# Kernel optimization log

Measured on AMD Instinct MI355X. Metric: run time of the kernel, lower is better.

## Reference

```python
import jax, jax.numpy as jnp
import numpy as np

D = 256          # out_feats
H = 4            # n_heads
DH = D // H      # per-head feats
S = 8192         # number of snapshots (segments)
PER = 32         # edges (selected papers) per snapshot
E = S * PER      # total edges
NP = 200000      # number of papers
ST = 10          # snapshot_types (embedding has ST+1 rows, padding_idx=-1)
SLOPE = 0.01     # LeakyReLU negative slope (torch default)


def setup_inputs() -> dict:
    key = jax.random.key(0)
    ks = jax.random.split(key, 20)
    sc = 1.0 / np.sqrt(D)
    papers = jax.random.normal(ks[0], (NP, D), dtype=jnp.float32)
    snapshots = jax.random.normal(ks[1], (S, D), dtype=jnp.float32)
    cur_snapshot_types = jax.random.randint(ks[2], (S,), 0, ST + 1, dtype=jnp.int32)
    is_cite = jax.random.randint(ks[3], (NP,), 0, 2, dtype=jnp.int32)
    selected_indicator = jax.random.randint(ks[4], (E,), 0, NP, dtype=jnp.int64)
    # contiguous sorted segment ids, PER edges per snapshot (matches valid_num_nodes)
    index = jnp.repeat(jnp.arange(S, dtype=jnp.int32), PER)
    # linear layers (torch Linear: y = x @ W.T + b)
    W_src = jax.random.normal(ks[5], (D, D), dtype=jnp.float32) * sc
    b_src = jnp.zeros((D,), dtype=jnp.float32)
    W_dst = jax.random.normal(ks[6], (D, D), dtype=jnp.float32) * sc
    b_dst = jnp.zeros((D,), dtype=jnp.float32)
    W_out = jax.random.normal(ks[7], (D, D), dtype=jnp.float32) * sc
    b_out = jnp.zeros((D,), dtype=jnp.float32)
    # node attr embeddings (2 rows, padding_idx=0 -> row 0 zero)
    emb_cite = jax.random.normal(ks[8], (2, D), dtype=jnp.float32).at[0].set(0.0)
    emb_ref = jax.random.normal(ks[9], (2, D), dtype=jnp.float32).at[0].set(0.0)
    emb_target = jax.random.normal(ks[10], (2, D), dtype=jnp.float32).at[0].set(0.0)
    # snapshot type embedding (ST+1 rows, padding_idx=-1 -> last row zero)
    snapshot_emb = jax.random.normal(ks[11], (ST + 1, D), dtype=jnp.float32).at[-1].set(0.0)
    # attention vectors, xavier_normal with relu gain
    gain = np.sqrt(2.0)
    std = gain * np.sqrt(2.0 / (H * DH + 1))
    attn = jax.random.normal(ks[12], (1, H, DH), dtype=jnp.float32) * std
    attn_t = jax.random.normal(ks[13], (1, H, DH), dtype=jnp.float32) * std
    return {
        "papers": papers, "snapshots": snapshots,
        "W_src": W_src, "b_src": b_src, "W_dst": W_dst, "b_dst": b_dst,
        "W_out": W_out, "b_out": b_out,
        "emb_cite": emb_cite, "emb_ref": emb_ref, "emb_target": emb_target,
        "snapshot_emb": snapshot_emb, "attn": attn, "attn_t": attn_t,
        "cur_snapshot_types": cur_snapshot_types, "is_cite": is_cite,
        "selected_indicator": selected_indicator, "index": index,
    }


def _leaky(x):
    return jnp.where(x >= 0, x, SLOPE * x)


def reference(papers, snapshots, W_src, b_src, W_dst, b_dst, W_out, b_out,
              emb_cite, emb_ref, emb_target, snapshot_emb, attn, attn_t,
              cur_snapshot_types, is_cite, selected_indicator, index):
    # gather src papers per edge: [E, D]
    h_src = papers[selected_indicator]
    feat_src = (h_src @ W_src.T + b_src).reshape(-1, H, DH)          # [E,H,DH]
    ic = is_cite[selected_indicator]
    # original uses 'is_cite' indices for all three attr embeddings (faithful)
    src_type_h = (emb_cite[ic] + emb_ref[ic] + emb_target[ic]).reshape(-1, H, DH)
    dst_type_h = snapshot_emb[cur_snapshot_types].reshape(-1, H, DH)  # [S,H,DH]
    feat_dst = (snapshots @ W_dst.T + b_dst).reshape(-1, H, DH)[index]  # [E,H,DH]
    # per-edge attention logits
    e = (_leaky(feat_src + feat_dst) * attn).sum(axis=-1)             # [E,H]
    et = (_leaky(src_type_h + dst_type_h[index]) * attn_t).sum(axis=-1)
    e = e + et
    # segment (edge) softmax over destination snapshots
    m = jax.lax.stop_gradient(jax.ops.segment_max(e, index, num_segments=S))
    ex = jnp.exp(e - m[index])
    den = jax.ops.segment_sum(ex, index, num_segments=S)
    a = (ex / den[index])[..., None]                                  # [E,H,1]
    # weighted segment-sum aggregation
    x = feat_src * a
    sum_out = jax.ops.segment_sum(x, index, num_segments=S).reshape(S, D)
    return sum_out @ W_out.T + b_out
```

## Files before the change

### kernel.cpp

```cpp
#include <hip/hip_runtime.h>
#include <hip/hip_fp16.h>
#include <type_traits>

#define NSNAP 8192
#define PER 32
#define SLOPE 0.01f

using half8   = __attribute__((ext_vector_type(8))) _Float16;
using floatx4 = __attribute__((ext_vector_type(4))) float;

__device__ __forceinline__ float leaky(float x) { return x >= 0.f ? x : SLOPE * x; }

__device__ __forceinline__ unsigned pack2(float a, float b) {
    __half2 h = __floats2half2_rn(a, b);
    return *reinterpret_cast<unsigned*>(&h);
}

__global__ __launch_bounds__(256) void pack_w(const float* __restrict__ W,
                                              _Float16* __restrict__ Wh) {
    const int i = blockIdx.x * 256 + threadIdx.x;
    const float4 v = *(const float4*)(W + (long)i * 4);
    *(uint2*)(Wh + (long)i * 4) = make_uint2(pack2(v.x, v.y), pack2(v.z, v.w));
}

template <typename AT, typename OT>
__global__ __launch_bounds__(256) void gemm_nt(const AT* __restrict__ A,
                                               const float* __restrict__ W,
                                               const float* __restrict__ bias,
                                               OT* __restrict__ Cout, int M) {
    constexpr int LDA = 40;
    __shared__ _Float16 Asl[128 * LDA];
    __shared__ _Float16 Wsl[128 * LDA];

    const int m0 = blockIdx.x * 128;
    const int n0 = blockIdx.y * 128;
    const int tid = threadIdx.x;
    const int lane = tid & 63;
    const int wave = tid >> 6;
    const int wm = (wave & 1) * 64;
    const int wn = (wave >> 1) * 64;
    const int l15 = lane & 15;
    const int quad = lane >> 4;

    floatx4 acc[4][4];
#pragma unroll
    for (int i = 0; i < 4; i++)
#pragma unroll
        for (int j = 0; j < 4; j++) acc[i][j] = (floatx4)0.f;

    for (int k0 = 0; k0 < 256; k0 += 32) {
        __syncthreads();
#pragma unroll
        for (int it = 0; it < 4; ++it) {
            const int idx = tid + it * 256;
            const int row = idx >> 3;
            const int c4 = idx & 7;
            long gm = (long)m0 + row;
            if (gm >= M) gm = M - 1;
            if constexpr (std::is_same_v<AT, float>) {
                const float4 v = *(const float4*)(A + gm * 256 + k0 + c4 * 4);
                *(uint2*)(&Asl[row * LDA + c4 * 4]) = make_uint2(pack2(v.x, v.y), pack2(v.z, v.w));
            } else {
                const uint2 v = *(const uint2*)(A + gm * 256 + k0 + c4 * 4);
                *(uint2*)(&Asl[row * LDA + c4 * 4]) = v;
            }
            const float4 w = *(const float4*)(W + (long)(n0 + row) * 256 + k0 + c4 * 4);
            *(uint2*)(&Wsl[row * LDA + c4 * 4]) = make_uint2(pack2(w.x, w.y), pack2(w.z, w.w));
        }
        __syncthreads();

        half8 af[4], bf[4];
#pragma unroll
        for (int i = 0; i < 4; i++)
            af[i] = *reinterpret_cast<const half8*>(&Asl[(wm + i * 16 + l15) * LDA + quad * 8]);
#pragma unroll
        for (int j = 0; j < 4; j++)
            bf[j] = *reinterpret_cast<const half8*>(&Wsl[(wn + j * 16 + l15) * LDA + quad * 8]);
#pragma unroll
        for (int i = 0; i < 4; i++)
#pragma unroll
            for (int j = 0; j < 4; j++)
                acc[i][j] = __builtin_amdgcn_mfma_f32_16x16x32_f16(af[i], bf[j], acc[i][j], 0, 0, 0);
    }

#pragma unroll
    for (int j = 0; j < 4; j++) {
        const int gcol = n0 + wn + j * 16 + l15;
        const float bv = bias[gcol];
#pragma unroll
        for (int i = 0; i < 4; i++) {
            const int rbase = m0 + wm + i * 16 + quad * 4;
#pragma unroll
            for (int r = 0; r < 4; r++) {
                const int grow = rbase + r;
                if (grow < M) {
                    const float v = acc[i][j][r] + bv;
                    if constexpr (std::is_same_v<OT, __half>)
                        Cout[(long)grow * 256 + gcol] = __float2half(v);
                    else
                        Cout[(long)grow * 256 + gcol] = v;
                }
            }
        }
    }
}

__global__ __launch_bounds__(256, 2) void fused_attn(
    const float* __restrict__ papers, const _Float16* __restrict__ Wh,
    const float* __restrict__ b_src, const float* __restrict__ F,
    const float* __restrict__ emb_cite, const float* __restrict__ emb_ref,
    const float* __restrict__ emb_target, const float* __restrict__ snap_emb,
    const float* __restrict__ attn, const float* __restrict__ attn_t,
    const int* __restrict__ types, const int* __restrict__ is_cite,
    const int* __restrict__ sel, __half* __restrict__ SO) {
    constexpr int LDA = 40;
    __shared__ _Float16 Asl[64 * LDA];
    __shared__ _Float16 Wsl[256 * LDA];
    __shared__ int ic_l[64];

    const int tid = threadIdx.x;
    const int lane = tid & 63;
    const int wave = tid >> 6;
    const int l15 = lane & 15;
    const int quad = lane >> 4;
    const int sbase = blockIdx.x * 2;
    const int ebase = blockIdx.x * 64;

    if (tid < 64) ic_l[tid] = is_cite[sel[ebase + tid]];

    const int arow_idx = tid >> 2;
    const int ac8 = tid & 3;
    const long arow = (long)sel[ebase + arow_idx];

    floatx4 acc[4][4];
#pragma unroll
    for (int i = 0; i < 4; i++)
#pragma unroll
        for (int j = 0; j < 4; j++) acc[i][j] = (floatx4)0.f;

    for (int k0 = 0; k0 < 256; k0 += 32) {
        __syncthreads();
        const float4 a0 = *(const float4*)(papers + arow * 256 + k0 + ac8 * 8);
        const float4 a1 = *(const float4*)(papers + arow * 256 + k0 + ac8 * 8 + 4);
        *(uint4*)(&Asl[arow_idx * LDA + ac8 * 8]) =
            make_uint4(pack2(a0.x, a0.y), pack2(a0.z, a0.w), pack2(a1.x, a1.y), pack2(a1.z, a1.w));
#pragma unroll
        for (int it = 0; it < 4; ++it) {
            const int task = tid + it * 256;
            const int n = task >> 2;
            const int c = task & 3;
            *(uint4*)(&Wsl[n * LDA + c * 8]) = *(const uint4*)(Wh + n * 256 + k0 + c * 8);
        }
        __syncthreads();

        half8 af[4], bf[4];
#pragma unroll
        for (int i = 0; i < 4; i++)
            af[i] = *reinterpret_cast<const half8*>(&Asl[(i * 16 + l15) * LDA + quad * 8]);
#pragma unroll
        for (int j = 0; j < 4; j++)
            bf[j] = *reinterpret_cast<const half8*>(&Wsl[(64 * wave + j * 16 + l15) * LDA + quad * 8]);
#pragma unroll
        for (int i = 0; i < 4; i++)
#pragma unroll
            for (int j = 0; j < 4; j++)
                acc[i][j] = __builtin_amdgcn_mfma_f32_16x16x32_f16(af[i], bf[j], acc[i][j], 0, 0, 0);
    }

    float bsrc_j[4], attn_j[4], F0_j[4], F1_j[4];
#pragma unroll
    for (int j = 0; j < 4; j++) {
        const int col = 64 * wave + j * 16 + l15;
        bsrc_j[j] = b_src[col];
        attn_j[j] = attn[col];
        F0_j[j] = F[(long)sbase * 256 + col];
        F1_j[j] = F[(long)(sbase + 1) * 256 + col];
    }
#pragma unroll
    for (int i = 0; i < 4; i++)
#pragma unroll
        for (int j = 0; j < 4; j++)
#pragma unroll
            for (int r = 0; r < 4; r++) acc[i][j][r] += bsrc_j[j];

    const int D = 64 * wave + lane;
    const float at_d = attn_t[D];
    const float src0 = emb_cite[D] + emb_ref[D] + emb_target[D];
    const float src1 = emb_cite[256 + D] + emb_ref[256 + D] + emb_target[256 + D];
    float et[2][2];
#pragma unroll
    for (int sn = 0; sn < 2; sn++) {
        const float dstt = snap_emb[types[sbase + sn] * 256 + D];
        float p0 = leaky(src0 + dstt) * at_d;
        float p1 = leaky(src1 + dstt) * at_d;
#pragma unroll
        for (int off = 32; off; off >>= 1) {
            p0 += __shfl_xor(p0, off);
            p1 += __shfl_xor(p1, off);
        }
        et[sn][0] = p0;
        et[sn][1] = p1;
    }

    float lg[4][4];
#pragma unroll
    for (int i = 0; i < 4; i++) {
        const int sn = i >> 1;
#pragma unroll
        for (int r = 0; r < 4; r++) {
            float p = 0.f;
#pragma unroll
            for (int j = 0; j < 4; j++)
                p += leaky(acc[i][j][r] + (sn == 0 ? F0_j[j] : F1_j[j])) * attn_j[j];
#pragma unroll
            for (int off = 1; off <= 8; off <<= 1) p += __shfl_xor(p, off);
            const int row = i * 16 + quad * 4 + r;
            lg[i][r] = p + et[sn][ic_l[row]];
        }
    }

    float aw[4][4];
#pragma unroll
    for (int sn = 0; sn < 2; sn++) {
        float m = -3.4e38f;
#pragma unroll
        for (int ii = 0; ii < 2; ii++)
#pragma unroll
            for (int r = 0; r < 4; r++) m = fmaxf(m, lg[sn * 2 + ii][r]);
        m = fmaxf(m, __shfl_xor(m, 16));
        m = fmaxf(m, __shfl_xor(m, 32));
        float den = 0.f;
#pragma unroll
        for (int ii = 0; ii < 2; ii++)
#pragma unroll
            for (int r = 0; r < 4; r++) {
                const float ex = __expf(lg[sn * 2 + ii][r] - m);
                aw[sn * 2 + ii][r] = ex;
                den += ex;
            }
        den += __shfl_xor(den, 16);
        den += __shfl_xor(den, 32);
        const float inv = 1.f / den;
#pragma unroll
        for (int ii = 0; ii < 2; ii++)
#pragma unroll
            for (int r = 0; r < 4; r++) aw[sn * 2 + ii][r] *= inv;
    }

#pragma unroll
    for (int sn = 0; sn < 2; sn++) {
#pragma unroll
        for (int j = 0; j < 4; j++) {
            float o = 0.f;
#pragma unroll
            for (int ii = 0; ii < 2; ii++)
#pragma unroll
                for (int r = 0; r < 4; r++) o += aw[sn * 2 + ii][r] * acc[sn * 2 + ii][j][r];
            o += __shfl_xor(o, 16);
            o += __shfl_xor(o, 32);
            if (quad == sn)
                SO[(long)(sbase + sn) * 256 + 64 * wave + j * 16 + l15] = __float2half(o);
        }
    }
}

extern "C" void kernel_launch(void* const* d_in, const int* in_sizes, int n_in,
                              void* d_out, int out_size, void* d_ws, size_t ws_size,
                              hipStream_t stream) {
    const float* papers     = (const float*)d_in[0];
    const float* snapshots  = (const float*)d_in[1];
    const float* W_src      = (const float*)d_in[2];
    const float* b_src      = (const float*)d_in[3];
    const float* W_dst      = (const float*)d_in[4];
    const float* b_dst      = (const float*)d_in[5];
    const float* W_out      = (const float*)d_in[6];
    const float* b_out      = (const float*)d_in[7];
    const float* emb_cite   = (const float*)d_in[8];
    const float* emb_ref    = (const float*)d_in[9];
    const float* emb_target = (const float*)d_in[10];
    const float* snap_emb   = (const float*)d_in[11];
    const float* attn       = (const float*)d_in[12];
    const float* attn_t     = (const float*)d_in[13];
    const int* types        = (const int*)d_in[14];
    const int* is_cite      = (const int*)d_in[15];
    const int* sel          = (const int*)d_in[16];

    char* ws = (char*)d_ws;
    float*     F    = (float*)ws;
    __half*    SO   = (__half*)(ws + 8388608);
    _Float16*  Wh   = (_Float16*)(ws + 12582912);

    pack_w<<<64, 256, 0, stream>>>(W_src, Wh);
    gemm_nt<float, float><<<dim3(64, 2), 256, 0, stream>>>(snapshots, W_dst, b_dst, F, NSNAP);
    fused_attn<<<NSNAP / 2, 256, 0, stream>>>(papers, Wh, b_src, F, emb_cite, emb_ref,
                                              emb_target, snap_emb, attn, attn_t, types,
                                              is_cite, sel, SO);
    gemm_nt<__half, float><<<dim3(64, 2), 256, 0, stream>>>(SO, W_out, b_out, (float*)d_out, NSNAP);
}
```

Measured before the change: 414.3 us.

## Prepack W_src in MFMA fragment order and stage full A tile once

```diff
diff --git a/kernel.cpp b/kernel.cpp
--- a/kernel.cpp
+++ b/kernel.cpp
@@ -16,11 +16,18 @@
     return *reinterpret_cast<unsigned*>(&h);
 }
 
-__global__ __launch_bounds__(256) void pack_w(const float* __restrict__ W,
-                                              _Float16* __restrict__ Wh) {
-    const int i = blockIdx.x * 256 + threadIdx.x;
-    const float4 v = *(const float4*)(W + (long)i * 4);
-    *(uint2*)(Wh + (long)i * 4) = make_uint2(pack2(v.x, v.y), pack2(v.z, v.w));
+__global__ __launch_bounds__(256) void pack_w_frag(const float* __restrict__ W,
+                                                   _Float16* __restrict__ Wh) {
+    const int t = blockIdx.x * 256 + threadIdx.x;
+    const int lane = t & 63;
+    const int wj = (t >> 6) & 15;
+    const int k0 = t >> 10;
+    const int n = (wj >> 2) * 64 + (wj & 3) * 16 + (lane & 15);
+    const int k = k0 * 32 + (lane >> 4) * 8;
+    const float4 v0 = *(const float4*)(W + (long)n * 256 + k);
+    const float4 v1 = *(const float4*)(W + (long)n * 256 + k + 4);
+    *(uint4*)(Wh + (long)t * 8) =
+        make_uint4(pack2(v0.x, v0.y), pack2(v0.z, v0.w), pack2(v1.x, v1.y), pack2(v1.z, v1.w));
 }
 
 template <typename AT, typename OT>
@@ -113,9 +120,7 @@
     const float* __restrict__ attn, const float* __restrict__ attn_t,
     const int* __restrict__ types, const int* __restrict__ is_cite,
     const int* __restrict__ sel, __half* __restrict__ SO) {
-    constexpr int LDA = 40;
-    __shared__ _Float16 Asl[64 * LDA];
-    __shared__ _Float16 Wsl[256 * LDA];
+    __shared__ _Float16 Asl[64 * 256];
     __shared__ int ic_l[64];
 
     const int tid = threadIdx.x;
@@ -128,9 +133,24 @@
 
     if (tid < 64) ic_l[tid] = is_cite[sel[ebase + tid]];
 
-    const int arow_idx = tid >> 2;
-    const int ac8 = tid & 3;
-    const long arow = (long)sel[ebase + arow_idx];
+    {
+        const int r = tid >> 2;
+        const int q0 = tid & 3;
+        const long arow = (long)sel[ebase + r];
+        const float* src = papers + arow * 256 + q0 * 64;
+        const int i = r >> 4;
+        const int rl = r & 15;
+#pragma unroll
+        for (int m = 0; m < 8; m++) {
+            const float4 a0 = *(const float4*)(src + m * 8);
+            const float4 a1 = *(const float4*)(src + m * 8 + 4);
+            const int c8 = q0 * 8 + m;
+            const int addr8 = (c8 >> 2) * 256 + i * 64 + (c8 & 3) * 16 + rl;
+            *(uint4*)(&Asl[addr8 * 8]) = make_uint4(pack2(a0.x, a0.y), pack2(a0.z, a0.w),
+                                                    pack2(a1.x, a1.y), pack2(a1.z, a1.w));
+        }
+    }
+    __syncthreads();
 
     floatx4 acc[4][4];
 #pragma unroll
@@ -138,28 +158,14 @@
 #pragma unroll
         for (int j = 0; j < 4; j++) acc[i][j] = (floatx4)0.f;
 
-    for (int k0 = 0; k0 < 256; k0 += 32) {
-        __syncthreads();
-        const float4 a0 = *(const float4*)(papers + arow * 256 + k0 + ac8 * 8);
-        const float4 a1 = *(const float4*)(papers + arow * 256 + k0 + ac8 * 8 + 4);
-        *(uint4*)(&Asl[arow_idx * LDA + ac8 * 8]) =
-            make_uint4(pack2(a0.x, a0.y), pack2(a0.z, a0.w), pack2(a1.x, a1.y), pack2(a1.z, a1.w));
-#pragma unroll
-        for (int it = 0; it < 4; ++it) {
-            const int task = tid + it * 256;
-            const int n = task >> 2;
-            const int c = task & 3;
-            *(uint4*)(&Wsl[n * LDA + c * 8]) = *(const uint4*)(Wh + n * 256 + k0 + c * 8);
-        }
-        __syncthreads();
-
+    for (int k0 = 0; k0 < 8; k0++) {
         half8 af[4], bf[4];
 #pragma unroll
         for (int i = 0; i < 4; i++)
-            af[i] = *reinterpret_cast<const half8*>(&Asl[(i * 16 + l15) * LDA + quad * 8]);
+            af[i] = *reinterpret_cast<const half8*>(&Asl[(k0 * 256 + i * 64 + lane) * 8]);
 #pragma unroll
         for (int j = 0; j < 4; j++)
-            bf[j] = *reinterpret_cast<const half8*>(&Wsl[(64 * wave + j * 16 + l15) * LDA + quad * 8]);
+            bf[j] = *reinterpret_cast<const half8*>(Wh + ((k0 * 16 + wave * 4 + j) * 64 + lane) * 8);
 #pragma unroll
         for (int i = 0; i < 4; i++)
 #pragma unroll
@@ -290,7 +296,7 @@
     __half*    SO   = (__half*)(ws + 8388608);
     _Float16*  Wh   = (_Float16*)(ws + 12582912);
 
-    pack_w<<<64, 256, 0, stream>>>(W_src, Wh);
+    pack_w_frag<<<128, 256, 0, stream>>>(W_src, Wh);
     gemm_nt<float, float><<<dim3(64, 2), 256, 0, stream>>>(snapshots, W_dst, b_dst, F, NSNAP);
     fused_attn<<<NSNAP / 2, 256, 0, stream>>>(papers, Wh, b_src, F, emb_cite, emb_ref,
                                               emb_target, snap_emb, attn, attn_t, types,
```

New measurement: 404.8 us. 1.02x faster.
